# Performance work log

Hardware: AMD Instinct MI355X
Metric: run time of the kernel (lower is better)

The kernel has to match this reference:

```python
import jax, jax.numpy as jnp
import numpy as np

B, N, D = 8, 2048, 1024


def setup_inputs() -> dict:
    key = jax.random.key(0)
    k = jax.random.split(key, 6)
    scale = 1.0 / np.sqrt(D)
    x = jax.random.normal(k[0], (B, N, D), dtype=jnp.float32)
    attention_mask = jax.random.randint(k[1], (B, N, N), 0, 2, dtype=jnp.int32)
    W_qkv = jax.random.normal(k[2], (D, 3 * D), dtype=jnp.float32) * scale
    b_qkv = jax.random.normal(k[3], (3 * D,), dtype=jnp.float32) * 0.01
    W_out = jax.random.normal(k[4], (D, D), dtype=jnp.float32) * scale
    b_out = jax.random.normal(k[5], (D,), dtype=jnp.float32) * 0.01
    return {"x": x, "attention_mask": attention_mask, "W_qkv": W_qkv,
            "b_qkv": b_qkv, "W_out": W_out, "b_out": b_out}


def reference(x, attention_mask, W_qkv, b_qkv, W_out, b_out):
    # QKV projection: [B,N,3D]
    qkv = jnp.einsum('bnd,de->bne', x, W_qkv) + b_qkv
    Q, K, V = jnp.split(qkv, 3, axis=-1)
    inv_sqrt_d = jnp.float32(1.0 / np.sqrt(D))
    # naive full [B,N,N] attention scores
    scores = jnp.einsum('bqd,bkd->bqk', Q, K) * inv_sqrt_d
    w = jax.nn.softmax(scores, axis=-1)
    # masked_fill(mask == 0, -1e20) then renormalize (module applies softmax
    # again over the masked weights; dropout is identity in eval mode)
    w = jnp.where(attention_mask == 0, jnp.float32(-1e20), w)
    w = jax.nn.softmax(w, axis=-1)
    out = jnp.einsum('bqk,bkd->bqd', w, V)
    return jnp.einsum('bnd,de->bne', out, W_out) + b_out
```

## Files before the change

### kernel.cpp

```cpp
#include <hip/hip_runtime.h>
#include <hip/hip_bf16.h>

typedef __attribute__((ext_vector_type(8))) short short8;
typedef __attribute__((ext_vector_type(4))) float floatx4;
typedef __attribute__((ext_vector_type(8))) int intx8;

#define AS_GLOBAL(p) ((const __attribute__((address_space(1))) void*)(p))
#define AS_LOCAL(p)  ((__attribute__((address_space(3))) void*)(p))

__device__ __forceinline__ float b2f(unsigned short u) {
    union { unsigned int u; float f; } c; c.u = ((unsigned int)u) << 16; return c.f;
}
__device__ __forceinline__ unsigned short f2b(float f) {
    union { float f; unsigned int u; } c; c.f = f;
    unsigned int u = c.u;
    unsigned int r = (u + 0x7fffu + ((u >> 16) & 1u)) >> 16;
    return (unsigned short)r;
}
__device__ __forceinline__ unsigned char f2fp8(float v) {
    return (unsigned char)(__builtin_amdgcn_cvt_pk_fp8_f32(v, v, 0, false) & 0xff);
}

__global__ __launch_bounds__(256) void cast_x(
    const float* __restrict__ in, unsigned short* __restrict__ xbf,
    unsigned int* __restrict__ xf8, int n4) {
    int i = blockIdx.x * 256 + threadIdx.x;
    if (i >= n4) return;
    float4 v = ((const float4*)in)[i];
    ushort4 o;
    o.x = f2b(v.x); o.y = f2b(v.y); o.z = f2b(v.z); o.w = f2b(v.w);
    ((ushort4*)xbf)[i] = o;
    int p = __builtin_amdgcn_cvt_pk_fp8_f32(v.x, v.y, 0, false);
    p = __builtin_amdgcn_cvt_pk_fp8_f32(v.z, v.w, p, true);
    xf8[i] = (unsigned int)p;
}

__global__ __launch_bounds__(256) void transpose_f32_bf16(
    const float* __restrict__ in, unsigned short* __restrict__ out, int R, int C) {
    __shared__ float t[32][33];
    int c0 = blockIdx.x * 32, r0 = blockIdx.y * 32;
    int tx = threadIdx.x, ty = threadIdx.y;
#pragma unroll
    for (int k = 0; k < 32; k += 8)
        t[ty + k][tx] = in[(size_t)(r0 + ty + k) * C + c0 + tx];
    __syncthreads();
#pragma unroll
    for (int k = 0; k < 32; k += 8)
        out[(size_t)(c0 + ty + k) * R + r0 + tx] = f2b(t[tx][ty + k]);
}

__global__ __launch_bounds__(256) void transpose_f32_fp8_qk(
    const float* __restrict__ in, unsigned char* __restrict__ out) {
    __shared__ float t[32][33];
    int c0 = blockIdx.x * 32, r0 = blockIdx.y * 32;
    int tx = threadIdx.x, ty = threadIdx.y;
#pragma unroll
    for (int k = 0; k < 32; k += 8)
        t[ty + k][tx] = in[(size_t)(r0 + ty + k) * 3072 + c0 + tx];
    __syncthreads();
#pragma unroll
    for (int k = 0; k < 32; k += 8)
        out[(size_t)(c0 + ty + k) * 1024 + r0 + tx] = f2fp8(t[tx][ty + k]);
}

__global__ __launch_bounds__(256) void cast_wv(
    const float* __restrict__ in, unsigned short* __restrict__ out) {
    int i = blockIdx.x * 256 + threadIdx.x;
    int d = i >> 8, rem = (i & 255) * 4;
    float4 v = *(const float4*)&in[(size_t)d * 3072 + 2048 + rem];
    ushort4 o;
    o.x = f2b(v.x); o.y = f2b(v.y); o.z = f2b(v.z); o.w = f2b(v.w);
    *(ushort4*)&out[(size_t)d * 1024 + rem] = o;
}

__global__ __launch_bounds__(256) void bvo_kernel(
    const unsigned short* __restrict__ WoT, const float* __restrict__ bqkv,
    const float* __restrict__ bout, float* __restrict__ bvo) {
    int wv = threadIdx.x >> 6, lane = threadIdx.x & 63;
    int e = blockIdx.x * 4 + wv;
    const unsigned short* row = WoT + (size_t)e * 1024;
    float s = 0.f;
    for (int h = lane; h < 1024; h += 64) s += b2f(row[h]) * bqkv[2048 + h];
#pragma unroll
    for (int o = 32; o; o >>= 1) s += __shfl_xor(s, o);
    if (lane == 0) bvo[e] = s + bout[e];
}

__global__ __launch_bounds__(256) void transpose_bf16_64(
    const unsigned short* __restrict__ in, unsigned short* __restrict__ out,
    int ldin, int ldout, long long sIn, long long sOut) {
    __shared__ unsigned short t[64][66];
    int b = blockIdx.z;
    const unsigned short* inb = in + (size_t)b * sIn;
    unsigned short* outb = out + (size_t)b * sOut;
    int c0 = blockIdx.x * 64, r0 = blockIdx.y * 64;
    int tx = threadIdx.x, ty = threadIdx.y;
#pragma unroll
    for (int k = 0; k < 64; k += 8) {
        int r = ty + k;
        *(ushort2*)&t[r][2 * tx] =
            *(const ushort2*)&inb[(size_t)(r0 + r) * ldin + c0 + 2 * tx];
    }
    __syncthreads();
#pragma unroll
    for (int k = 0; k < 64; k += 8) {
        int c = ty + k;
        ushort2 v; v.x = t[2 * tx][c]; v.y = t[2 * tx + 1][c];
        *(ushort2*)&outb[(size_t)(c0 + c) * ldout + r0 + 2 * tx] = v;
    }
}

__global__ __launch_bounds__(256) void softmax2_kernel(
    unsigned short* __restrict__ S, const int* __restrict__ mask) {
    const int N = 2048;
    int wv = threadIdx.x >> 6, lane = threadIdx.x & 63;
    size_t row = (size_t)blockIdx.x * 4 + wv;
    unsigned short* srow = S + row * N;
    const int* mrow = mask + row * N;

    float e1[32];
    float l = 0.f;
#pragma unroll
    for (int i = 0; i < 4; ++i) {
        uint4 raw = ((const uint4*)srow)[lane + 64 * i];
        unsigned v[4] = { raw.x, raw.y, raw.z, raw.w };
#pragma unroll
        for (int j = 0; j < 4; ++j) {
            float a = b2f((unsigned short)(v[j] & 0xffff));
            float bb = b2f((unsigned short)(v[j] >> 16));
            float ea = __expf(a), eb = __expf(bb);
            e1[i * 8 + 2 * j] = ea; e1[i * 8 + 2 * j + 1] = eb;
            l += ea + eb;
        }
    }
#pragma unroll
    for (int o = 32; o; o >>= 1) l += __shfl_xor(l, o);
    float invl = 1.0f / l;

    float e2[32];
    float z = 0.f;
#pragma unroll
    for (int i = 0; i < 4; ++i) {
        uint4 m0 = ((const uint4*)mrow)[2 * (lane + 64 * i)];
        uint4 m1 = ((const uint4*)mrow)[2 * (lane + 64 * i) + 1];
        int mk[8] = { (int)m0.x, (int)m0.y, (int)m0.z, (int)m0.w,
                      (int)m1.x, (int)m1.y, (int)m1.z, (int)m1.w };
#pragma unroll
        for (int j = 0; j < 8; ++j) {
            float w1 = e1[i * 8 + j] * invl;
            float e = mk[j] ? __expf(w1) : 0.0f;
            e2[i * 8 + j] = e; z += e;
        }
    }
#pragma unroll
    for (int o = 32; o; o >>= 1) z += __shfl_xor(z, o);
    float invz = (z > 0.f) ? 1.0f / z : 0.0f;
    float fallback = 1.0f / N;
#pragma unroll
    for (int i = 0; i < 4; ++i) {
        float p[8];
#pragma unroll
        for (int j = 0; j < 8; ++j)
            p[j] = (z > 0.f) ? e2[i * 8 + j] * invz : fallback;
        uint4 o;
        o.x = (unsigned)f2b(p[0]) | ((unsigned)f2b(p[1]) << 16);
        o.y = (unsigned)f2b(p[2]) | ((unsigned)f2b(p[3]) << 16);
        o.z = (unsigned)f2b(p[4]) | ((unsigned)f2b(p[5]) << 16);
        o.w = (unsigned)f2b(p[6]) | ((unsigned)f2b(p[7]) << 16);
        ((uint4*)srow)[lane + 64 * i] = o;
    }
}

template <int TAG, bool BIAS, bool OUTF32>
__global__ __launch_bounds__(256) void gemm_bt(
    const unsigned short* __restrict__ A, int ldA, long long strideA,
    const unsigned short* __restrict__ B, int ldB, long long strideB,
    void* __restrict__ C, int ldC, long long strideC,
    const float* __restrict__ bias, float scale, int K) {
    __shared__ __align__(16) unsigned short lds[2 * 128 * 64];
    unsigned short* At = lds;
    unsigned short* Bt = lds + 128 * 64;

    int b = blockIdx.z;
    const unsigned short* Ab = A + (size_t)b * strideA;
    const unsigned short* Bb = B + (size_t)b * strideB;
    int tn0 = blockIdx.x * 128;
    int tm0 = blockIdx.y * 128;
    int tid = threadIdx.x;
    int wave = tid >> 6, lane = tid & 63;
    int lm = lane & 15, q = lane >> 4;
    int wm = (wave >> 1) * 64, wn = (wave & 1) * 64;

    int srow = lane >> 3;
    int sblk = lane & 7;

    floatx4 acc[4][4] = {};

    for (int k0 = 0; k0 < K; k0 += 64) {
        __syncthreads();
#pragma unroll
        for (int i = 0; i < 4; ++i) {
            int chunk = wave * 4 + i;
            int r = chunk * 8 + srow;
            int blk = sblk ^ (r & 7);
            const unsigned short* ga = Ab + (size_t)(tm0 + r) * ldA + (k0 + blk * 8);
            __builtin_amdgcn_global_load_lds(AS_GLOBAL(ga), AS_LOCAL(At + chunk * 512), 16, 0, 0);
            const unsigned short* gb = Bb + (size_t)(tn0 + r) * ldB + (k0 + blk * 8);
            __builtin_amdgcn_global_load_lds(AS_GLOBAL(gb), AS_LOCAL(Bt + chunk * 512), 16, 0, 0);
        }
        __syncthreads();
#pragma unroll
        for (int kk = 0; kk < 2; ++kk) {
            short8 af[4], bf[4];
#pragma unroll
            for (int mt = 0; mt < 4; ++mt) {
                int r = wm + mt * 16 + lm;
                af[mt] = *(const short8*)(At + r * 64 + (((kk * 4 + q) ^ (r & 7)) * 8));
            }
#pragma unroll
            for (int nt = 0; nt < 4; ++nt) {
                int r = wn + nt * 16 + lm;
                bf[nt] = *(const short8*)(Bt + r * 64 + (((kk * 4 + q) ^ (r & 7)) * 8));
            }
#pragma unroll
            for (int mt = 0; mt < 4; ++mt)
#pragma unroll
                for (int nt = 0; nt < 4; ++nt)
                    acc[mt][nt] = __builtin_amdgcn_mfma_f32_16x16x32_bf16(
                        af[mt], bf[nt], acc[mt][nt], 0, 0, 0);
        }
    }

    float biasv[4];
#pragma unroll
    for (int nt = 0; nt < 4; ++nt)
        biasv[nt] = BIAS ? bias[tn0 + wn + nt * 16 + lm] : 0.0f;
#pragma unroll
    for (int mt = 0; mt < 4; ++mt) {
#pragma unroll
        for (int nt = 0; nt < 4; ++nt) {
            int gm = tm0 + wm + mt * 16 + q * 4;
            int gn = tn0 + wn + nt * 16 + lm;
#pragma unroll
            for (int r = 0; r < 4; ++r) {
                float v = acc[mt][nt][r] * scale;
                if (BIAS) v += biasv[nt];
                size_t idx = (size_t)b * strideC + (size_t)(gm + r) * ldC + gn;
                if (OUTF32) ((float*)C)[idx] = v;
                else        ((unsigned short*)C)[idx] = f2b(v);
            }
        }
    }
}

template <int TAG, bool BIAS, bool OUTFP8>
__global__ __launch_bounds__(256) void gemm_f8_bt(
    const unsigned char* __restrict__ A, int ldA, long long strideA,
    const unsigned char* __restrict__ B, int ldB, long long strideB,
    void* __restrict__ C, int ldC, long long strideC,
    const float* __restrict__ bias, float scale, int K) {
    __shared__ __align__(16) unsigned char lds[2 * 128 * 128];
    unsigned char* At = lds;
    unsigned char* Bt = lds + 128 * 128;

    int b = blockIdx.z;
    const unsigned char* Ab = A + (size_t)b * strideA;
    const unsigned char* Bb = B + (size_t)b * strideB;
    int tn0 = blockIdx.x * 128;
    int tm0 = blockIdx.y * 128;
    int tid = threadIdx.x;
    int wave = tid >> 6, lane = tid & 63;
    int lm = lane & 15, q = lane >> 4;
    int q2 = q * 2;
    int wm = (wave >> 1) * 64, wn = (wave & 1) * 64;

    int srow = lane >> 3;
    int sblk = lane & 7;

    floatx4 acc[4][4] = {};

    for (int k0 = 0; k0 < K; k0 += 128) {
        __syncthreads();
#pragma unroll
        for (int i = 0; i < 4; ++i) {
            int chunk = wave * 4 + i;
            int r = chunk * 8 + srow;
            int blk = sblk ^ (r & 7);
            const unsigned char* ga = Ab + (size_t)(tm0 + r) * ldA + (k0 + blk * 16);
            __builtin_amdgcn_global_load_lds(AS_GLOBAL(ga), AS_LOCAL(At + chunk * 1024), 16, 0, 0);
            const unsigned char* gb = Bb + (size_t)(tn0 + r) * ldB + (k0 + blk * 16);
            __builtin_amdgcn_global_load_lds(AS_GLOBAL(gb), AS_LOCAL(Bt + chunk * 1024), 16, 0, 0);
        }
        __syncthreads();
        intx8 af[4], bf[4];
#pragma unroll
        for (int mt = 0; mt < 4; ++mt) {
            int r = wm + mt * 16 + lm;
            const unsigned char* base = At + r * 128;
            int4 lo = *(const int4*)(base + ((q2 ^ (r & 7)) << 4));
            int4 hi = *(const int4*)(base + (((q2 + 1) ^ (r & 7)) << 4));
            af[mt][0] = lo.x; af[mt][1] = lo.y; af[mt][2] = lo.z; af[mt][3] = lo.w;
            af[mt][4] = hi.x; af[mt][5] = hi.y; af[mt][6] = hi.z; af[mt][7] = hi.w;
        }
#pragma unroll
        for (int nt = 0; nt < 4; ++nt) {
            int r = wn + nt * 16 + lm;
            const unsigned char* base = Bt + r * 128;
            int4 lo = *(const int4*)(base + ((q2 ^ (r & 7)) << 4));
            int4 hi = *(const int4*)(base + (((q2 + 1) ^ (r & 7)) << 4));
            bf[nt][0] = lo.x; bf[nt][1] = lo.y; bf[nt][2] = lo.z; bf[nt][3] = lo.w;
            bf[nt][4] = hi.x; bf[nt][5] = hi.y; bf[nt][6] = hi.z; bf[nt][7] = hi.w;
        }
#pragma unroll
        for (int mt = 0; mt < 4; ++mt)
#pragma unroll
            for (int nt = 0; nt < 4; ++nt)
                acc[mt][nt] = __builtin_amdgcn_mfma_scale_f32_16x16x128_f8f6f4(
                    af[mt], bf[nt], acc[mt][nt], 0, 0,
                    0, 0x7f7f7f7f, 0, 0x7f7f7f7f);
    }

    float biasv[4];
#pragma unroll
    for (int nt = 0; nt < 4; ++nt)
        biasv[nt] = BIAS ? bias[tn0 + wn + nt * 16 + lm] : 0.0f;
#pragma unroll
    for (int mt = 0; mt < 4; ++mt) {
#pragma unroll
        for (int nt = 0; nt < 4; ++nt) {
            int gm = tm0 + wm + mt * 16 + q * 4;
            int gn = tn0 + wn + nt * 16 + lm;
#pragma unroll
            for (int r = 0; r < 4; ++r) {
                float v = acc[mt][nt][r] * scale;
                if (BIAS) v += biasv[nt];
                size_t idx = (size_t)b * strideC + (size_t)(gm + r) * ldC + gn;
                if (OUTFP8) ((unsigned char*)C)[idx] = f2fp8(v);
                else        ((unsigned short*)C)[idx] = f2b(v);
            }
        }
    }
}

extern "C" void kernel_launch(void* const* d_in, const int* in_sizes, int n_in,
                              void* d_out, int out_size, void* d_ws, size_t ws_size,
                              hipStream_t stream) {
    const float* x    = (const float*)d_in[0];
    const int*   mask = (const int*)d_in[1];
    const float* Wqkv = (const float*)d_in[2];
    const float* bqkv = (const float*)d_in[3];
    const float* Wout = (const float*)d_in[4];
    const float* bout = (const float*)d_in[5];
    float* out = (float*)d_out;

    char* w = (char*)d_ws;
    unsigned short* x_bf  = (unsigned short*)(w);
    unsigned char*  x_f8  = (unsigned char*)(w + 33554432);
    unsigned char*  QKf8  = (unsigned char*)(w + 50331648);
    unsigned short* Vp    = (unsigned short*)(w + 83886080);
    unsigned short* VpT   = (unsigned short*)(w + 117440512);
    unsigned short* S     = (unsigned short*)(w + 150994944);
    unsigned char*  WqkT8 = (unsigned char*)(w + 218103808);
    unsigned short* WoT   = (unsigned short*)(w + 220200960);
    unsigned short* Wv_bf = (unsigned short*)(w + 222298112);
    unsigned short* WvoT  = (unsigned short*)(w + 224395264);
    float*          bvo   = (float*)(w + 226492416);

    cast_x<<<16384, 256, 0, stream>>>(x, x_bf, (unsigned int*)x_f8, 4194304);
    transpose_f32_fp8_qk<<<dim3(64, 32), dim3(32, 8), 0, stream>>>(Wqkv, WqkT8);
    transpose_f32_bf16<<<dim3(32, 32), dim3(32, 8), 0, stream>>>(Wout, WoT, 1024, 1024);
    cast_wv<<<1024, 256, 0, stream>>>(Wqkv, Wv_bf);
    bvo_kernel<<<256, 256, 0, stream>>>(WoT, bqkv, bout, bvo);

    gemm_bt<4, false, false><<<dim3(8, 8, 1), 256, 0, stream>>>(
        WoT, 1024, 0, Wv_bf, 1024, 0, WvoT, 1024, 0, nullptr, 1.0f, 1024);

    gemm_f8_bt<0, true, true><<<dim3(16, 128, 1), 256, 0, stream>>>(
        x_f8, 1024, 0, WqkT8, 1024, 0, QKf8, 2048, 0, bqkv, 1.0f, 1024);

    gemm_bt<5, true, false><<<dim3(8, 128, 1), 256, 0, stream>>>(
        x_bf, 1024, 0, WvoT, 1024, 0, Vp, 1024, 0, bvo, 1.0f, 1024);

    transpose_bf16_64<<<dim3(16, 32, 8), dim3(32, 8), 0, stream>>>(
        Vp, VpT, 1024, 2048, 2048LL * 1024, 1024LL * 2048);

    gemm_f8_bt<1, false, false><<<dim3(16, 16, 8), 256, 0, stream>>>(
        QKf8, 2048, 2048LL * 2048, QKf8 + 1024, 2048, 2048LL * 2048,
        S, 2048, 2048LL * 2048, nullptr, 0.03125f, 1024);

    softmax2_kernel<<<4096, 256, 0, stream>>>(S, mask);

    gemm_bt<2, false, true><<<dim3(8, 16, 8), 256, 0, stream>>>(
        S, 2048, 2048LL * 2048, VpT, 2048, 1024LL * 2048,
        out, 1024, 2048LL * 1024, nullptr, 1.0f, 2048);
}
```

Baseline: 568.5 us.

## Fuse V transpose into GEMM epilogue and remap workgroups across XCDs

The V projection GEMM now writes its output already transposed. It stages the tile through swizzled LDS and does vectorized 16-byte stores, which removes the separate transpose kernel and the round trip of the intermediate Vp buffer through global memory. All GEMMs switch to a flat 1D grid with a workgroup remap, (flat&7)*(grid/8)+(flat>>3), so consecutive tiles land on the same XCD for better L2 locality. The remap assumes the grid size is a multiple of 8 and that tile counts are powers of two.

```diff
diff --git a/kernel.cpp b/kernel.cpp
--- a/kernel.cpp
+++ b/kernel.cpp
@@ -86,30 +86,6 @@
     if (lane == 0) bvo[e] = s + bout[e];
 }
 
-__global__ __launch_bounds__(256) void transpose_bf16_64(
-    const unsigned short* __restrict__ in, unsigned short* __restrict__ out,
-    int ldin, int ldout, long long sIn, long long sOut) {
-    __shared__ unsigned short t[64][66];
-    int b = blockIdx.z;
-    const unsigned short* inb = in + (size_t)b * sIn;
-    unsigned short* outb = out + (size_t)b * sOut;
-    int c0 = blockIdx.x * 64, r0 = blockIdx.y * 64;
-    int tx = threadIdx.x, ty = threadIdx.y;
-#pragma unroll
-    for (int k = 0; k < 64; k += 8) {
-        int r = ty + k;
-        *(ushort2*)&t[r][2 * tx] =
-            *(const ushort2*)&inb[(size_t)(r0 + r) * ldin + c0 + 2 * tx];
-    }
-    __syncthreads();
-#pragma unroll
-    for (int k = 0; k < 64; k += 8) {
-        int c = ty + k;
-        ushort2 v; v.x = t[2 * tx][c]; v.y = t[2 * tx + 1][c];
-        *(ushort2*)&outb[(size_t)(c0 + c) * ldout + r0 + 2 * tx] = v;
-    }
-}
-
 __global__ __launch_bounds__(256) void softmax2_kernel(
     unsigned short* __restrict__ S, const int* __restrict__ mask) {
     const int N = 2048;
@@ -171,7 +147,7 @@
     }
 }
 
-template <int TAG, bool BIAS, bool OUTF32>
+template <int TAG, bool BIAS, int OUT, int XS, int YS>
 __global__ __launch_bounds__(256) void gemm_bt(
     const unsigned short* __restrict__ A, int ldA, long long strideA,
     const unsigned short* __restrict__ B, int ldB, long long strideB,
@@ -181,11 +157,16 @@
     unsigned short* At = lds;
     unsigned short* Bt = lds + 128 * 64;
 
-    int b = blockIdx.z;
-    const unsigned short* Ab = A + (size_t)b * strideA;
-    const unsigned short* Bb = B + (size_t)b * strideB;
-    int tn0 = blockIdx.x * 128;
-    int tm0 = blockIdx.y * 128;
+    unsigned flat = blockIdx.x;
+    unsigned wg = (flat & 7u) * (gridDim.x >> 3) + (flat >> 3);
+    int bx = wg & ((1u << XS) - 1u);
+    int by = (wg >> XS) & ((1u << YS) - 1u);
+    int bz = wg >> (XS + YS);
+
+    const unsigned short* Ab = A + (size_t)bz * strideA;
+    const unsigned short* Bb = B + (size_t)bz * strideB;
+    int tn0 = bx * 128;
+    int tm0 = by * 128;
     int tid = threadIdx.x;
     int wave = tid >> 6, lane = tid & 63;
     int lm = lane & 15, q = lane >> 4;
@@ -235,6 +216,38 @@
 #pragma unroll
     for (int nt = 0; nt < 4; ++nt)
         biasv[nt] = BIAS ? bias[tn0 + wn + nt * 16 + lm] : 0.0f;
+
+    if (OUT == 2) {
+        __syncthreads();
+        unsigned short* T = lds;
+#pragma unroll
+        for (int mt = 0; mt < 4; ++mt)
+#pragma unroll
+            for (int nt = 0; nt < 4; ++nt) {
+                int n = wn + nt * 16 + lm;
+                int m0 = wm + mt * 16 + q * 4;
+                int col = m0 ^ ((n & 15) << 3);
+                ushort4 pv;
+                float v0 = acc[mt][nt][0] * scale; if (BIAS) v0 += biasv[nt];
+                float v1 = acc[mt][nt][1] * scale; if (BIAS) v1 += biasv[nt];
+                float v2 = acc[mt][nt][2] * scale; if (BIAS) v2 += biasv[nt];
+                float v3 = acc[mt][nt][3] * scale; if (BIAS) v3 += biasv[nt];
+                pv.x = f2b(v0); pv.y = f2b(v1); pv.z = f2b(v2); pv.w = f2b(v3);
+                *(ushort4*)&T[n * 128 + col] = pv;
+            }
+        __syncthreads();
+        unsigned short* Cb = (unsigned short*)C + (size_t)(tm0 >> 11) * strideC + (tm0 & 2047);
+#pragma unroll
+        for (int r8 = 0; r8 < 8; ++r8) {
+            int idx = tid + 256 * r8;
+            int d = idx >> 4, c = idx & 15;
+            int cs = (c ^ (d & 15)) << 3;
+            short8 v = *(const short8*)&T[d * 128 + cs];
+            *(short8*)&Cb[(size_t)(tn0 + d) * ldC + c * 8] = v;
+        }
+        return;
+    }
+
 #pragma unroll
     for (int mt = 0; mt < 4; ++mt) {
 #pragma unroll
@@ -245,15 +258,15 @@
             for (int r = 0; r < 4; ++r) {
                 float v = acc[mt][nt][r] * scale;
                 if (BIAS) v += biasv[nt];
-                size_t idx = (size_t)b * strideC + (size_t)(gm + r) * ldC + gn;
-                if (OUTF32) ((float*)C)[idx] = v;
-                else        ((unsigned short*)C)[idx] = f2b(v);
+                size_t idx = (size_t)bz * strideC + (size_t)(gm + r) * ldC + gn;
+                if (OUT == 1) ((float*)C)[idx] = v;
+                else          ((unsigned short*)C)[idx] = f2b(v);
             }
         }
     }
 }
 
-template <int TAG, bool BIAS, bool OUTFP8>
+template <int TAG, bool BIAS, bool OUTFP8, int XS, int YS>
 __global__ __launch_bounds__(256) void gemm_f8_bt(
     const unsigned char* __restrict__ A, int ldA, long long strideA,
     const unsigned char* __restrict__ B, int ldB, long long strideB,
@@ -263,11 +276,16 @@
     unsigned char* At = lds;
     unsigned char* Bt = lds + 128 * 128;
 
-    int b = blockIdx.z;
-    const unsigned char* Ab = A + (size_t)b * strideA;
-    const unsigned char* Bb = B + (size_t)b * strideB;
-    int tn0 = blockIdx.x * 128;
-    int tm0 = blockIdx.y * 128;
+    unsigned flat = blockIdx.x;
+    unsigned wg = (flat & 7u) * (gridDim.x >> 3) + (flat >> 3);
+    int bx = wg & ((1u << XS) - 1u);
+    int by = (wg >> XS) & ((1u << YS) - 1u);
+    int bz = wg >> (XS + YS);
+
+    const unsigned char* Ab = A + (size_t)bz * strideA;
+    const unsigned char* Bb = B + (size_t)bz * strideB;
+    int tn0 = bx * 128;
+    int tm0 = by * 128;
     int tid = threadIdx.x;
     int wave = tid >> 6, lane = tid & 63;
     int lm = lane & 15, q = lane >> 4;
@@ -334,7 +352,7 @@
             for (int r = 0; r < 4; ++r) {
                 float v = acc[mt][nt][r] * scale;
                 if (BIAS) v += biasv[nt];
-                size_t idx = (size_t)b * strideC + (size_t)(gm + r) * ldC + gn;
+                size_t idx = (size_t)bz * strideC + (size_t)(gm + r) * ldC + gn;
                 if (OUTFP8) ((unsigned char*)C)[idx] = f2fp8(v);
                 else        ((unsigned short*)C)[idx] = f2b(v);
             }
@@ -357,7 +375,6 @@
     unsigned short* x_bf  = (unsigned short*)(w);
     unsigned char*  x_f8  = (unsigned char*)(w + 33554432);
     unsigned char*  QKf8  = (unsigned char*)(w + 50331648);
-    unsigned short* Vp    = (unsigned short*)(w + 83886080);
     unsigned short* VpT   = (unsigned short*)(w + 117440512);
     unsigned short* S     = (unsigned short*)(w + 150994944);
     unsigned char*  WqkT8 = (unsigned char*)(w + 218103808);
@@ -372,25 +389,22 @@
     cast_wv<<<1024, 256, 0, stream>>>(Wqkv, Wv_bf);
     bvo_kernel<<<256, 256, 0, stream>>>(WoT, bqkv, bout, bvo);
 
-    gemm_bt<4, false, false><<<dim3(8, 8, 1), 256, 0, stream>>>(
+    gemm_bt<4, false, 0, 3, 3><<<64, 256, 0, stream>>>(
         WoT, 1024, 0, Wv_bf, 1024, 0, WvoT, 1024, 0, nullptr, 1.0f, 1024);
 
-    gemm_f8_bt<0, true, true><<<dim3(16, 128, 1), 256, 0, stream>>>(
+    gemm_f8_bt<0, true, true, 4, 7><<<2048, 256, 0, stream>>>(
         x_f8, 1024, 0, WqkT8, 1024, 0, QKf8, 2048, 0, bqkv, 1.0f, 1024);
 
-    gemm_bt<5, true, false><<<dim3(8, 128, 1), 256, 0, stream>>>(
-        x_bf, 1024, 0, WvoT, 1024, 0, Vp, 1024, 0, bvo, 1.0f, 1024);
-
-    transpose_bf16_64<<<dim3(16, 32, 8), dim3(32, 8), 0, stream>>>(
-        Vp, VpT, 1024, 2048, 2048LL * 1024, 1024LL * 2048);
-
-    gemm_f8_bt<1, false, false><<<dim3(16, 16, 8), 256, 0, stream>>>(
+    gemm_bt<5, true, 2, 3, 7><<<1024, 256, 0, stream>>>(
+        x_bf, 1024, 0, WvoT, 1024, 0, VpT, 2048, 1024LL * 2048, bvo, 1.0f, 1024);
+
+    gemm_f8_bt<1, false, false, 4, 4><<<2048, 256, 0, stream>>>(
         QKf8, 2048, 2048LL * 2048, QKf8 + 1024, 2048, 2048LL * 2048,
         S, 2048, 2048LL * 2048, nullptr, 0.03125f, 1024);
 
     softmax2_kernel<<<4096, 256, 0, stream>>>(S, mask);
 
-    gemm_bt<2, false, true><<<dim3(8, 16, 8), 256, 0, stream>>>(
+    gemm_bt<2, false, 1, 3, 4><<<1024, 256, 0, stream>>>(
         S, 2048, 2048LL * 2048, VpT, 2048, 1024LL * 2048,
         out, 1024, 2048LL * 1024, nullptr, 1.0f, 2048);
 }
```

Result: faster. 530.2 us (-6.7%).
